# Kernel tuning notes

Hardware: AMD Instinct MI355X
Metric: run time of the kernel (lower is better)

Reference implementation:

```python
import jax, jax.numpy as jnp
import numpy as np

B, G, D, H, KD, E = 64, 512, 128, 8, 16, 128
NS = 20  # num_station


def _init_w(key, shape):
    stdv = 1.0 / np.sqrt(shape[-1]).astype(np.float32)
    return jax.random.uniform(key, shape, jnp.float32, -stdv, stdv)


def setup_inputs() -> dict:
    key = jax.random.key(0)
    ks = jax.random.split(key, 12)
    return {
        "q": jax.random.normal(ks[0], (B, G, D), jnp.float32),
        "h": jax.random.normal(ks[1], (B, G, D), jnp.float32),
        "W_query_depot": _init_w(ks[2], (H, D, KD)),
        "W_key_custom": _init_w(ks[3], (H, D, KD)),
        "W_val_custom": _init_w(ks[4], (H, D, KD)),
        "W_query_station": _init_w(ks[5], (H, D, KD)),
        "W_key_other": _init_w(ks[6], (H, D, KD)),
        "W_val_other": _init_w(ks[7], (H, D, KD)),
        "W_query_custom": _init_w(ks[8], (H, D, KD)),
        "W_key_all": _init_w(ks[9], (H, D, KD)),
        "W_val_all": _init_w(ks[10], (H, D, KD)),
        "W_out": _init_w(ks[11], (H, KD, E)),
        "num_station": NS,
    }


def _mha_block(q_seg, h_seg, Wq, Wk, Wv, norm):
    # q_seg: [B, Nq, D], h_seg: [B, Nk, D]; weights: [H, D, KD]
    Q = jnp.einsum('bqd,hdk->hbqk', q_seg, Wq)
    K = jnp.einsum('bnd,hdk->hbnk', h_seg, Wk)
    V = jnp.einsum('bnd,hdk->hbnk', h_seg, Wv)
    attn = jax.nn.softmax(norm * jnp.einsum('hbqk,hbnk->hbqn', Q, K), axis=-1)
    return jnp.einsum('hbqn,hbnk->hbqk', attn, V)  # [H, B, Nq, KD]


def reference(q, h, W_query_depot, W_key_custom, W_val_custom,
              W_query_station, W_key_other, W_val_other,
              W_query_custom, W_key_all, W_val_all, W_out, num_station):
    ns = num_station
    norm = 1.0 / np.sqrt(W_query_depot.shape[-1]).astype(np.float32)
    h_custom = h[:, 1 + ns:]                                        # customers
    h_other = jnp.concatenate([h[:, :1], h[:, 1 + ns:]], axis=1)    # depot + customers
    heads_depot = _mha_block(q[:, :1], h_custom,
                             W_query_depot, W_key_custom, W_val_custom, norm)
    heads_station = _mha_block(q[:, 1:1 + ns], h_other,
                               W_query_station, W_key_other, W_val_other, norm)
    heads_custom = _mha_block(q[:, 1 + ns:], h,
                              W_query_custom, W_key_all, W_val_all, norm)
    heads = jnp.concatenate([heads_depot, heads_station, heads_custom], axis=2)
    # final projection: mm([B*G, H*KD], [H*KD, E])
    return jnp.einsum('hbgk,hke->bge', heads, W_out)
```

## Files before the change

### kernel.cpp

```cpp
#include <hip/hip_runtime.h>
#include <hip/hip_bf16.h>

namespace {

typedef _Float16 v4h __attribute__((ext_vector_type(4)));
typedef __fp16   h2  __attribute__((ext_vector_type(2)));
typedef float    v4f __attribute__((ext_vector_type(4)));

constexpr int B = 64, G = 512, D = 128, H = 8, KD = 16, NS = 20;
constexpr float NORM = 0.25f;
constexpr float L2E  = 1.44269504088896f;
constexpr float MFIX = 16.0f;
constexpr int KP = 20;
constexpr int VP = 520;

constexpr size_t SZr(int r) { return (size_t)B * H * r * 16; }
constexpr size_t OFF_Q    = 0;
constexpr size_t OFF_K0   = OFF_Q  + SZr(512);
constexpr size_t OFF_V0   = OFF_K0 + SZr(491);
constexpr size_t OFF_K1   = OFF_V0 + SZr(491);
constexpr size_t OFF_V1   = OFF_K1 + SZr(492);
constexpr size_t OFF_K2   = OFF_V1 + SZr(492);
constexpr size_t OFF_V2   = OFF_K2 + SZr(512);
constexpr size_t OFF_FRAG = OFF_V2 + SZr(512);

__device__ __forceinline__ v4f mfma16(v4h a, v4h b, v4f c) {
  return __builtin_amdgcn_mfma_f32_16x16x16f16(a, b, c, 0, 0, 0);
}
__device__ __forceinline__ v4h cvt4(float4 v) {
  h2 a = __builtin_amdgcn_cvt_pkrtz(v.x, v.y);
  h2 b = __builtin_amdgcn_cvt_pkrtz(v.z, v.w);
  return v4h{(_Float16)a[0], (_Float16)a[1], (_Float16)b[0], (_Float16)b[1]};
}
__device__ __forceinline__ v4h cvtacc(v4f v) {
  h2 a = __builtin_amdgcn_cvt_pkrtz(v[0], v[1]);
  h2 b = __builtin_amdgcn_cvt_pkrtz(v[2], v[3]);
  return v4h{(_Float16)a[0], (_Float16)a[1], (_Float16)b[0], (_Float16)b[1]};
}
__device__ __forceinline__ void pexp(v4f s0, v4f s1, v4h& p0, v4h& p1) {
  h2 e01 = __builtin_amdgcn_cvt_pkrtz(__builtin_amdgcn_exp2f(s0[0]),
                                      __builtin_amdgcn_exp2f(s0[1]));
  h2 e23 = __builtin_amdgcn_cvt_pkrtz(__builtin_amdgcn_exp2f(s0[2]),
                                      __builtin_amdgcn_exp2f(s0[3]));
  h2 e45 = __builtin_amdgcn_cvt_pkrtz(__builtin_amdgcn_exp2f(s1[0]),
                                      __builtin_amdgcn_exp2f(s1[1]));
  h2 e67 = __builtin_amdgcn_cvt_pkrtz(__builtin_amdgcn_exp2f(s1[2]),
                                      __builtin_amdgcn_exp2f(s1[3]));
  p0 = {(_Float16)e01[0], (_Float16)e01[1], (_Float16)e23[0], (_Float16)e23[1]};
  p1 = {(_Float16)e45[0], (_Float16)e45[1], (_Float16)e67[0], (_Float16)e67[1]};
}

__global__ __launch_bounds__(256)
void wprep_kernel(const float* __restrict__ Wkc, const float* __restrict__ Wvc,
                  const float* __restrict__ Wko, const float* __restrict__ Wvo,
                  const float* __restrict__ Wka, const float* __restrict__ Wva,
                  const float* __restrict__ Wqc, const float* __restrict__ Wqs,
                  const float* __restrict__ Wqd, _Float16* __restrict__ ws)
{
  const int m = blockIdx.x >> 3;
  const int h = blockIdx.x & 7;
  const float* W;
  float sc = 1.f;
  switch (m) {
    case 0: W = Wkc; break;  case 1: W = Wvc; break;
    case 2: W = Wko; break;  case 3: W = Wvo; break;
    case 4: W = Wka; break;  case 5: W = Wva; break;
    case 6: W = Wqc; sc = NORM * L2E; break;
    case 7: W = Wqs; sc = NORM * L2E; break;
    default: W = Wqd; sc = NORM * L2E; break;
  }
  #pragma unroll
  for (int it = 0; it < 2; ++it) {
    int idx = threadIdx.x + it * 256;
    int dc = idx >> 6, lane = idx & 63, g = lane >> 4, c = lane & 15;
    v4h out;
    #pragma unroll
    for (int i = 0; i < 4; ++i)
      out[i] = (_Float16)(W[((size_t)h * D + dc * 16 + 4 * g + i) * KD + c] * sc);
    *(v4h*)(ws + OFF_FRAG + (((size_t)(m * 8 + h) * 8 + dc) * 64 + lane) * 4) = out;
  }
}

__global__ __launch_bounds__(512)
void proj_kernel(const float* __restrict__ q, const float* __restrict__ hb,
                 _Float16* __restrict__ ws)
{
  const int rt   = blockIdx.x;
  const int b    = blockIdx.y;
  const int tid  = threadIdx.x;
  const int w    = tid >> 6;
  const int lane = tid & 63;
  const int g    = lane >> 4, c = lane & 15;

  __shared__ char ht[16384];

  #pragma unroll
  for (int i = 0; i < 4; ++i) {
    int idx = tid + i * 512, r = idx >> 5, jj = idx & 31;
    float4 v = ((const float4*)(hb + ((size_t)b * G + rt * 64 + r) * D))[jj];
    *(v4h*)(ht + r * 256 + ((8 * jj) ^ ((r & 7) << 4))) = cvt4(v);
  }
  __syncthreads();

  {
    constexpr size_t DOFF[6] = {OFF_K0, OFF_V0, OFF_K1, OFF_V1, OFF_K2, OFF_V2};
    constexpr int    DR[6]   = {491, 491, 492, 492, 512, 512};
    #pragma unroll
    for (int m = 0; m < 6; ++m) {
      v4h wf[8];
      #pragma unroll
      for (int dc = 0; dc < 8; ++dc)
        wf[dc] = *(const v4h*)(ws + OFF_FRAG +
                               (((size_t)(m * 8 + w) * 8 + dc) * 64 + lane) * 4);
      _Float16* dst = ws + DOFF[m] + (size_t)(b * H + w) * (DR[m] * 16);
      const int se = m >> 1;
      #pragma unroll
      for (int s = 0; s < 4; ++s) {
        v4f acc = {0.f, 0.f, 0.f, 0.f};
        #pragma unroll
        for (int dc = 0; dc < 8; ++dc) {
          const v4h a = *(const v4h*)(ht + (s * 16 + c) * 256 +
                                      ((32 * dc + 8 * g) ^ ((c & 7) << 4)));
          acc = mfma16(wf[dc], a, acc);
        }
        v4h out = cvtacc(acc);
        const int hr = rt * 64 + s * 16 + c;
        int n; bool valid;
        if (se == 2)      { n = hr; valid = true; }
        else if (se == 1) { valid = (hr == 0) || (hr >= 1 + NS);
                            n = (hr == 0) ? 0 : hr - NS; }
        else              { valid = (hr >= 1 + NS); n = hr - 1 - NS; }
        if (valid) *(v4h*)(dst + (size_t)n * 16 + 4 * g) = out;
      }
    }
  }

  __syncthreads();
  #pragma unroll
  for (int i = 0; i < 4; ++i) {
    int idx = tid + i * 512, r = idx >> 5, jj = idx & 31;
    float4 v = ((const float4*)(q + ((size_t)b * G + rt * 64 + r) * D))[jj];
    *(v4h*)(ht + r * 256 + ((8 * jj) ^ ((r & 7) << 4))) = cvt4(v);
  }
  __syncthreads();
  {
    auto qproj = [&](int mfrag, int s) -> v4h {
      v4h wf[8];
      #pragma unroll
      for (int dc = 0; dc < 8; ++dc)
        wf[dc] = *(const v4h*)(ws + OFF_FRAG +
                               (((size_t)(mfrag * 8 + w) * 8 + dc) * 64 + lane) * 4);
      v4f acc = {0.f, 0.f, 0.f, 0.f};
      #pragma unroll
      for (int dc = 0; dc < 8; ++dc) {
        const v4h a = *(const v4h*)(ht + (s * 16 + c) * 256 +
                                    ((32 * dc + 8 * g) ^ ((c & 7) << 4)));
        acc = mfma16(wf[dc], a, acc);
      }
      return cvtacc(acc);
    };
    _Float16* dst = ws + OFF_Q + (size_t)(b * H + w) * 512 * 16;
    #pragma unroll
    for (int s = 0; s < 4; ++s) {
      v4h out = qproj(6, s);
      if (rt == 0 && s < 2) {
        const int gq = s * 16 + c;
        v4h outS = qproj(7, s);
        if (s == 0) {
          v4h outD = qproj(8, 0);
          out = (gq == 0) ? outD : (gq <= NS ? outS : out);
        } else {
          out = (gq <= NS) ? outS : out;
        }
      }
      *(v4h*)(dst + (size_t)(rt * 64 + s * 16 + c) * 16 + 4 * g) = out;
    }
  }
}

struct SMA {
  _Float16  Kl[512 * KP];
  _Float16  Vt[16 * VP];
};

template<int SEG, bool PAIR>
__device__ __forceinline__ void attn_loop(const SMA& sm, int g, int c,
                                          v4h qfA, v4h qfB,
                                          v4f& oA, v4f& laA, v4f& oB, v4f& laB)
{
  constexpr int Ln  = SEG == 0 ? G - 1 - NS : SEG == 1 ? G - NS : G;
  constexpr int NCH = (Ln + 31) / 32;
  const _Float16* Kb = sm.Kl + c * KP + 4 * g;
  const _Float16* Vb = sm.Vt + c * VP + 4 * g;
  const v4f mc = {-MFIX, -MFIX, -MFIX, -MFIX};
  const v4h ones = {(_Float16)1.f, (_Float16)1.f, (_Float16)1.f, (_Float16)1.f};

  v4h k0 = *(const v4h*)(Kb);
  v4h k1 = *(const v4h*)(Kb + 16 * KP);
  v4f s0A = mfma16(k0, qfA, mc), s1A = mfma16(k1, qfA, mc);
  v4f s0B, s1B;
  if constexpr (PAIR) { s0B = mfma16(k0, qfB, mc); s1B = mfma16(k1, qfB, mc); }

  #pragma unroll
  for (int ch = 0; ch < NCH; ++ch) {
    const int nb = ch * 32;
    const v4h v0 = *(const v4h*)(Vb + nb);
    const v4h v1 = *(const v4h*)(Vb + nb + 16);
    v4f n0A, n1A, n0B, n1B;
    if (ch + 1 < NCH) {
      k0 = *(const v4h*)(Kb + (nb + 32) * KP);
      k1 = *(const v4h*)(Kb + (nb + 48) * KP);
      n0A = mfma16(k0, qfA, mc); n1A = mfma16(k1, qfA, mc);
      if constexpr (PAIR) { n0B = mfma16(k0, qfB, mc); n1B = mfma16(k1, qfB, mc); }
    }
    if constexpr ((Ln & 31) != 0) {
      if (ch == NCH - 1) {
        #pragma unroll
        for (int r = 0; r < 4; ++r) {
          if (nb + 4 * g + r >= Ln)      { s0A[r] = -1e30f; if constexpr (PAIR) s0B[r] = -1e30f; }
          if (nb + 16 + 4 * g + r >= Ln) { s1A[r] = -1e30f; if constexpr (PAIR) s1B[r] = -1e30f; }
        }
      }
    }
    v4h p0, p1;
    pexp(s0A, s1A, p0, p1);
    oA  = mfma16(v0, p0, oA);
    oA  = mfma16(v1, p1, oA);
    laA = mfma16(ones, p0, laA);
    laA = mfma16(ones, p1, laA);
    if constexpr (PAIR) {
      pexp(s0B, s1B, p0, p1);
      oB  = mfma16(v0, p0, oB);
      oB  = mfma16(v1, p1, oB);
      laB = mfma16(ones, p0, laB);
      laB = mfma16(ones, p1, laB);
      s0B = n0B; s1B = n1B;
    }
    s0A = n0A; s1A = n1A;
  }
}

template<int SEG>
__device__ __forceinline__ void seg_attn(int bid, const _Float16* __restrict__ ws,
                                         float* __restrict__ heads, SMA& sm)
{
  constexpr int Lq   = SEG == 0 ? 1 : SEG == 1 ? NS : G - 1 - NS;
  constexpr int QOFF = SEG == 0 ? 0 : SEG == 1 ? 1  : 1 + NS;
  constexpr int Ln   = SEG == 0 ? G - 1 - NS : SEG == 1 ? G - NS : G;
  constexpr int NQT  = (Lq + 15) / 16;
  constexpr size_t KO = SEG == 0 ? OFF_K0 : SEG == 1 ? OFF_K1 : OFF_K2;
  constexpr size_t VO = SEG == 0 ? OFF_V0 : SEG == 1 ? OFF_V1 : OFF_V2;

  const int hh   = bid >> 6;
  const int b    = bid & 63;
  const int tid  = threadIdx.x;
  const int w    = tid >> 6;
  const int lane = tid & 63;
  const int g    = lane >> 4, c = lane & 15;

  const _Float16* Kws = ws + KO + (size_t)(b * H + hh) * (Ln * 16);
  const _Float16* Vws = ws + VO + (size_t)(b * H + hh) * (Ln * 16);
  const _Float16* Qws = ws + OFF_Q + (size_t)(b * H + hh) * 512 * 16;

  {
    const int n = tid;
    float4 kA = ((const float4*)(Kws + (size_t)n * 16))[0];
    float4 kB = ((const float4*)(Kws + (size_t)n * 16))[1];
    v4h kk[4];
    *(float4*)&kk[0] = kA; *(float4*)&kk[2] = kB;
    #pragma unroll
    for (int i = 0; i < 4; ++i)
      *(v4h*)(sm.Kl + n * KP + 4 * i) = kk[i];
    float4 vA = ((const float4*)(Vws + (size_t)n * 16))[0];
    float4 vB = ((const float4*)(Vws + (size_t)n * 16))[1];
    _Float16 vt[16];
    *(float4*)&vt[0] = vA; *(float4*)&vt[8] = vB;
    #pragma unroll
    for (int k = 0; k < 16; ++k)
      sm.Vt[k * VP + n] = vt[k];
  }
  __syncthreads();

  #pragma unroll
  for (int ps = 0; ps < 2; ++ps) {
    const int t0 = w + 16 * ps, tB = w + 8 + 16 * ps;
    if (t0 >= NQT) continue;
    const bool hasB = tB < NQT;
    v4h qfA = *(const v4h*)(Qws + (size_t)(QOFF + t0 * 16 + c) * 16 + 4 * g);
    v4h qfB = hasB ? *(const v4h*)(Qws + (size_t)(QOFF + tB * 16 + c) * 16 + 4 * g) : qfA;
    v4f oA = {0.f,0.f,0.f,0.f}, laA = {0.f,0.f,0.f,0.f};
    v4f oB = {0.f,0.f,0.f,0.f}, laB = {0.f,0.f,0.f,0.f};
    if (hasB) attn_loop<SEG, true >(sm, g, c, qfA, qfB, oA, laA, oB, laB);
    else      attn_loop<SEG, false>(sm, g, c, qfA, qfA, oA, laA, oB, laB);
    {
      const float inv = 1.0f / laA[0];
      const int qloc = t0 * 16 + c;
      if (qloc < Lq) {
        float4 val = {oA[0]*inv, oA[1]*inv, oA[2]*inv, oA[3]*inv};
        *(float4*)(heads + ((size_t)b * G + QOFF + qloc) * 128 + hh * 16 + 4 * g) = val;
      }
    }
    if (hasB) {
      const float inv = 1.0f / laB[0];
      const int qloc = tB * 16 + c;
      if (qloc < Lq) {
        float4 val = {oB[0]*inv, oB[1]*inv, oB[2]*inv, oB[3]*inv};
        *(float4*)(heads + ((size_t)b * G + QOFF + qloc) * 128 + hh * 16 + 4 * g) = val;
      }
    }
  }
}

__global__ __launch_bounds__(512, 4)
void fused_attn(const _Float16* __restrict__ ws, float* __restrict__ heads)
{
  __shared__ SMA sm;
  const int bid = blockIdx.x;
  if (bid < 512)       seg_attn<2>(bid,        ws, heads, sm);
  else if (bid < 1024) seg_attn<1>(bid - 512,  ws, heads, sm);
  else                 seg_attn<0>(bid - 1024, ws, heads, sm);
}

__global__ __launch_bounds__(256)
void out_proj_kernel(float* __restrict__ data, const float* __restrict__ Wout)
{
  __shared__ _Float16 WlT[128 * 132];
  __shared__ _Float16 Ah [64 * 132];
  const int tid  = threadIdx.x;
  const int lane = tid & 63, w = tid >> 6;
  const int g = lane >> 4, c = lane & 15;
  const size_t rowbase = (size_t)blockIdx.x * 64;

  #pragma unroll
  for (int i = 0; i < 16; ++i) {
    int idx = tid + i * 256;
    int k = idx >> 5, c4 = (idx & 31) * 4;
    float4 v = ((const float4*)Wout)[idx];
    WlT[(c4 + 0) * 132 + k] = (_Float16)v.x;
    WlT[(c4 + 1) * 132 + k] = (_Float16)v.y;
    WlT[(c4 + 2) * 132 + k] = (_Float16)v.z;
    WlT[(c4 + 3) * 132 + k] = (_Float16)v.w;
  }
  #pragma unroll
  for (int i = 0; i < 8; ++i) {
    int idx = tid + i * 256;
    int r = idx >> 5, c4 = (idx & 31) * 4;
    float4 v = ((const float4*)(data + rowbase * 128))[idx];
    *(v4h*)(Ah + r * 132 + c4) = cvt4(v);
  }
  __syncthreads();

  v4h af[8];
  #pragma unroll
  for (int dc = 0; dc < 8; ++dc)
    af[dc] = *(const v4h*)(Ah + (w * 16 + c) * 132 + dc * 16 + 4 * g);
  #pragma unroll
  for (int ct = 0; ct < 8; ++ct) {
    v4f acc = {0.f, 0.f, 0.f, 0.f};
    #pragma unroll
    for (int dc = 0; dc < 8; ++dc) {
      const v4h bf = *(const v4h*)(WlT + (ct * 16 + c) * 132 + dc * 16 + 4 * g);
      acc = mfma16(af[dc], bf, acc);
    }
    #pragma unroll
    for (int r = 0; r < 4; ++r)
      data[(rowbase + w * 16 + 4 * g + r) * 128 + ct * 16 + c] = acc[r];
  }
}

}

extern "C" void kernel_launch(void* const* d_in, const int* in_sizes, int n_in,
                              void* d_out, int out_size, void* d_ws, size_t ws_size,
                              hipStream_t stream) {
  const float* q    = (const float*)d_in[0];
  const float* h    = (const float*)d_in[1];
  const float* Wqd  = (const float*)d_in[2];
  const float* Wkc  = (const float*)d_in[3];
  const float* Wvc  = (const float*)d_in[4];
  const float* Wqs  = (const float*)d_in[5];
  const float* Wko  = (const float*)d_in[6];
  const float* Wvo  = (const float*)d_in[7];
  const float* Wqc  = (const float*)d_in[8];
  const float* Wka  = (const float*)d_in[9];
  const float* Wva  = (const float*)d_in[10];
  const float* Wout = (const float*)d_in[11];
  float* out = (float*)d_out;
  _Float16* ws = (_Float16*)d_ws;

  wprep_kernel<<<72, 256, 0, stream>>>(Wkc, Wvc, Wko, Wvo, Wka, Wva,
                                       Wqc, Wqs, Wqd, ws);
  proj_kernel<<<dim3(8, B), 512, 0, stream>>>(q, h, ws);
  fused_attn<<<3 * B * H, 512, 0, stream>>>(ws, out);
  out_proj_kernel<<<G * B / 64, 256, 0, stream>>>(out, Wout);
}
```

Baseline: 78.63 us.

## Split projection grid finer and process four query tiles per K/V chunk

The projection kernel now runs 256-thread blocks over 32-row tiles and splits the 8 heads across two grid z-slices, which quadruples the block count. The cost is that each h/q tile is loaded and converted twice. The attention loop is restructured so each wave holds up to four query fragments and reads each K/V chunk from shared memory once for all of them. This replaces the paired A/B loop and its software-pipelined K prefetch, cutting LDS reads, but raises register pressure and drops the explicit prefetch.

```diff
diff --git a/kernel.cpp b/kernel.cpp
--- a/kernel.cpp
+++ b/kernel.cpp
@@ -81,23 +81,25 @@
   }
 }
 
-__global__ __launch_bounds__(512)
+__global__ __launch_bounds__(256)
 void proj_kernel(const float* __restrict__ q, const float* __restrict__ hb,
                  _Float16* __restrict__ ws)
 {
   const int rt   = blockIdx.x;
   const int b    = blockIdx.y;
+  const int hz   = blockIdx.z;
   const int tid  = threadIdx.x;
   const int w    = tid >> 6;
+  const int hh   = hz * 4 + w;
   const int lane = tid & 63;
   const int g    = lane >> 4, c = lane & 15;
 
-  __shared__ char ht[16384];
+  __shared__ char ht[8192];
 
   #pragma unroll
   for (int i = 0; i < 4; ++i) {
-    int idx = tid + i * 512, r = idx >> 5, jj = idx & 31;
-    float4 v = ((const float4*)(hb + ((size_t)b * G + rt * 64 + r) * D))[jj];
+    int idx = tid + i * 256, r = idx >> 5, jj = idx & 31;
+    float4 v = ((const float4*)(hb + ((size_t)b * G + rt * 32 + r) * D))[jj];
     *(v4h*)(ht + r * 256 + ((8 * jj) ^ ((r & 7) << 4))) = cvt4(v);
   }
   __syncthreads();
@@ -111,11 +113,11 @@
       #pragma unroll
       for (int dc = 0; dc < 8; ++dc)
         wf[dc] = *(const v4h*)(ws + OFF_FRAG +
-                               (((size_t)(m * 8 + w) * 8 + dc) * 64 + lane) * 4);
-      _Float16* dst = ws + DOFF[m] + (size_t)(b * H + w) * (DR[m] * 16);
+                               (((size_t)(m * 8 + hh) * 8 + dc) * 64 + lane) * 4);
+      _Float16* dst = ws + DOFF[m] + (size_t)(b * H + hh) * (DR[m] * 16);
       const int se = m >> 1;
       #pragma unroll
-      for (int s = 0; s < 4; ++s) {
+      for (int s = 0; s < 2; ++s) {
         v4f acc = {0.f, 0.f, 0.f, 0.f};
         #pragma unroll
         for (int dc = 0; dc < 8; ++dc) {
@@ -124,7 +126,7 @@
           acc = mfma16(wf[dc], a, acc);
         }
         v4h out = cvtacc(acc);
-        const int hr = rt * 64 + s * 16 + c;
+        const int hr = rt * 32 + s * 16 + c;
         int n; bool valid;
         if (se == 2)      { n = hr; valid = true; }
         else if (se == 1) { valid = (hr == 0) || (hr >= 1 + NS);
@@ -138,8 +140,8 @@
   __syncthreads();
   #pragma unroll
   for (int i = 0; i < 4; ++i) {
-    int idx = tid + i * 512, r = idx >> 5, jj = idx & 31;
-    float4 v = ((const float4*)(q + ((size_t)b * G + rt * 64 + r) * D))[jj];
+    int idx = tid + i * 256, r = idx >> 5, jj = idx & 31;
+    float4 v = ((const float4*)(q + ((size_t)b * G + rt * 32 + r) * D))[jj];
     *(v4h*)(ht + r * 256 + ((8 * jj) ^ ((r & 7) << 4))) = cvt4(v);
   }
   __syncthreads();
@@ -149,7 +151,7 @@
       #pragma unroll
       for (int dc = 0; dc < 8; ++dc)
         wf[dc] = *(const v4h*)(ws + OFF_FRAG +
-                               (((size_t)(mfrag * 8 + w) * 8 + dc) * 64 + lane) * 4);
+                               (((size_t)(mfrag * 8 + hh) * 8 + dc) * 64 + lane) * 4);
       v4f acc = {0.f, 0.f, 0.f, 0.f};
       #pragma unroll
       for (int dc = 0; dc < 8; ++dc) {
@@ -159,11 +161,11 @@
       }
       return cvtacc(acc);
     };
-    _Float16* dst = ws + OFF_Q + (size_t)(b * H + w) * 512 * 16;
-    #pragma unroll
-    for (int s = 0; s < 4; ++s) {
+    _Float16* dst = ws + OFF_Q + (size_t)(b * H + hh) * 512 * 16;
+    #pragma unroll
+    for (int s = 0; s < 2; ++s) {
       v4h out = qproj(6, s);
-      if (rt == 0 && s < 2) {
+      if (rt == 0) {
         const int gq = s * 16 + c;
         v4h outS = qproj(7, s);
         if (s == 0) {
@@ -173,7 +175,7 @@
           out = (gq <= NS) ? outS : out;
         }
       }
-      *(v4h*)(dst + (size_t)(rt * 64 + s * 16 + c) * 16 + 4 * g) = out;
+      *(v4h*)(dst + (size_t)(rt * 32 + s * 16 + c) * 16 + 4 * g) = out;
     }
   }
 }
@@ -183,63 +185,6 @@
   _Float16  Vt[16 * VP];
 };
 
-template<int SEG, bool PAIR>
-__device__ __forceinline__ void attn_loop(const SMA& sm, int g, int c,
-                                          v4h qfA, v4h qfB,
-                                          v4f& oA, v4f& laA, v4f& oB, v4f& laB)
-{
-  constexpr int Ln  = SEG == 0 ? G - 1 - NS : SEG == 1 ? G - NS : G;
-  constexpr int NCH = (Ln + 31) / 32;
-  const _Float16* Kb = sm.Kl + c * KP + 4 * g;
-  const _Float16* Vb = sm.Vt + c * VP + 4 * g;
-  const v4f mc = {-MFIX, -MFIX, -MFIX, -MFIX};
-  const v4h ones = {(_Float16)1.f, (_Float16)1.f, (_Float16)1.f, (_Float16)1.f};
-
-  v4h k0 = *(const v4h*)(Kb);
-  v4h k1 = *(const v4h*)(Kb + 16 * KP);
-  v4f s0A = mfma16(k0, qfA, mc), s1A = mfma16(k1, qfA, mc);
-  v4f s0B, s1B;
-  if constexpr (PAIR) { s0B = mfma16(k0, qfB, mc); s1B = mfma16(k1, qfB, mc); }
-
-  #pragma unroll
-  for (int ch = 0; ch < NCH; ++ch) {
-    const int nb = ch * 32;
-    const v4h v0 = *(const v4h*)(Vb + nb);
-    const v4h v1 = *(const v4h*)(Vb + nb + 16);
-    v4f n0A, n1A, n0B, n1B;
-    if (ch + 1 < NCH) {
-      k0 = *(const v4h*)(Kb + (nb + 32) * KP);
-      k1 = *(const v4h*)(Kb + (nb + 48) * KP);
-      n0A = mfma16(k0, qfA, mc); n1A = mfma16(k1, qfA, mc);
-      if constexpr (PAIR) { n0B = mfma16(k0, qfB, mc); n1B = mfma16(k1, qfB, mc); }
-    }
-    if constexpr ((Ln & 31) != 0) {
-      if (ch == NCH - 1) {
-        #pragma unroll
-        for (int r = 0; r < 4; ++r) {
-          if (nb + 4 * g + r >= Ln)      { s0A[r] = -1e30f; if constexpr (PAIR) s0B[r] = -1e30f; }
-          if (nb + 16 + 4 * g + r >= Ln) { s1A[r] = -1e30f; if constexpr (PAIR) s1B[r] = -1e30f; }
-        }
-      }
-    }
-    v4h p0, p1;
-    pexp(s0A, s1A, p0, p1);
-    oA  = mfma16(v0, p0, oA);
-    oA  = mfma16(v1, p1, oA);
-    laA = mfma16(ones, p0, laA);
-    laA = mfma16(ones, p1, laA);
-    if constexpr (PAIR) {
-      pexp(s0B, s1B, p0, p1);
-      oB  = mfma16(v0, p0, oB);
-      oB  = mfma16(v1, p1, oB);
-      laB = mfma16(ones, p0, laB);
-      laB = mfma16(ones, p1, laB);
-      s0B = n0B; s1B = n1B;
-    }
-    s0A = n0A; s1A = n1A;
-  }
-}
-
 template<int SEG>
 __device__ __forceinline__ void seg_attn(int bid, const _Float16* __restrict__ ws,
                                          float* __restrict__ heads, SMA& sm)
@@ -247,6 +192,7 @@
   constexpr int Lq   = SEG == 0 ? 1 : SEG == 1 ? NS : G - 1 - NS;
   constexpr int QOFF = SEG == 0 ? 0 : SEG == 1 ? 1  : 1 + NS;
   constexpr int Ln   = SEG == 0 ? G - 1 - NS : SEG == 1 ? G - NS : G;
+  constexpr int NCH  = (Ln + 31) / 32;
   constexpr int NQT  = (Lq + 15) / 16;
   constexpr size_t KO = SEG == 0 ? OFF_K0 : SEG == 1 ? OFF_K1 : OFF_K2;
   constexpr size_t VO = SEG == 0 ? OFF_V0 : SEG == 1 ? OFF_V1 : OFF_V2;
@@ -281,30 +227,57 @@
   }
   __syncthreads();
 
-  #pragma unroll
-  for (int ps = 0; ps < 2; ++ps) {
-    const int t0 = w + 16 * ps, tB = w + 8 + 16 * ps;
-    if (t0 >= NQT) continue;
-    const bool hasB = tB < NQT;
-    v4h qfA = *(const v4h*)(Qws + (size_t)(QOFF + t0 * 16 + c) * 16 + 4 * g);
-    v4h qfB = hasB ? *(const v4h*)(Qws + (size_t)(QOFF + tB * 16 + c) * 16 + 4 * g) : qfA;
-    v4f oA = {0.f,0.f,0.f,0.f}, laA = {0.f,0.f,0.f,0.f};
-    v4f oB = {0.f,0.f,0.f,0.f}, laB = {0.f,0.f,0.f,0.f};
-    if (hasB) attn_loop<SEG, true >(sm, g, c, qfA, qfB, oA, laA, oB, laB);
-    else      attn_loop<SEG, false>(sm, g, c, qfA, qfA, oA, laA, oB, laB);
-    {
-      const float inv = 1.0f / laA[0];
-      const int qloc = t0 * 16 + c;
+  v4h qf[4] = {};
+  #pragma unroll
+  for (int j = 0; j < 4; ++j) {
+    const int t = w + 8 * j;
+    if (t < NQT)
+      qf[j] = *(const v4h*)(Qws + (size_t)(QOFF + t * 16 + c) * 16 + 4 * g);
+  }
+
+  const _Float16* Kb = sm.Kl + c * KP + 4 * g;
+  const _Float16* Vb = sm.Vt + c * VP + 4 * g;
+  const v4f mc = {-MFIX, -MFIX, -MFIX, -MFIX};
+  const v4h ones = {(_Float16)1.f, (_Float16)1.f, (_Float16)1.f, (_Float16)1.f};
+  v4f o[4]  = {{0.f,0.f,0.f,0.f},{0.f,0.f,0.f,0.f},{0.f,0.f,0.f,0.f},{0.f,0.f,0.f,0.f}};
+  v4f la[4] = {{0.f,0.f,0.f,0.f},{0.f,0.f,0.f,0.f},{0.f,0.f,0.f,0.f},{0.f,0.f,0.f,0.f}};
+  #pragma unroll
+  for (int ch = 0; ch < NCH; ++ch) {
+    const int nb = ch * 32;
+    const v4h k0 = *(const v4h*)(Kb + nb * KP);
+    const v4h k1 = *(const v4h*)(Kb + (nb + 16) * KP);
+    const v4h v0 = *(const v4h*)(Vb + nb);
+    const v4h v1 = *(const v4h*)(Vb + nb + 16);
+    #pragma unroll
+    for (int j = 0; j < 4; ++j) {
+      if (w + 8 * j < NQT) {
+        v4f s0 = mfma16(k0, qf[j], mc);
+        v4f s1 = mfma16(k1, qf[j], mc);
+        if constexpr ((Ln & 31) != 0) {
+          if (ch == NCH - 1) {
+            #pragma unroll
+            for (int r = 0; r < 4; ++r) {
+              if (nb + 4 * g + r >= Ln)      s0[r] = -1e30f;
+              if (nb + 16 + 4 * g + r >= Ln) s1[r] = -1e30f;
+            }
+          }
+        }
+        v4h p0, p1;
+        pexp(s0, s1, p0, p1);
+        o[j]  = mfma16(v0, p0, o[j]);
+        o[j]  = mfma16(v1, p1, o[j]);
+        la[j] = mfma16(ones, p0, la[j]);
+        la[j] = mfma16(ones, p1, la[j]);
+      }
+    }
+  }
+  #pragma unroll
+  for (int j = 0; j < 4; ++j) {
+    if (w + 8 * j < NQT) {
+      const float inv = 1.0f / la[j][0];
+      const int qloc = (w + 8 * j) * 16 + c;
       if (qloc < Lq) {
-        float4 val = {oA[0]*inv, oA[1]*inv, oA[2]*inv, oA[3]*inv};
-        *(float4*)(heads + ((size_t)b * G + QOFF + qloc) * 128 + hh * 16 + 4 * g) = val;
-      }
-    }
-    if (hasB) {
-      const float inv = 1.0f / laB[0];
-      const int qloc = tB * 16 + c;
-      if (qloc < Lq) {
-        float4 val = {oB[0]*inv, oB[1]*inv, oB[2]*inv, oB[3]*inv};
+        float4 val = {o[j][0]*inv, o[j][1]*inv, o[j][2]*inv, o[j][3]*inv};
         *(float4*)(heads + ((size_t)b * G + QOFF + qloc) * 128 + hh * 16 + 4 * g) = val;
       }
     }
@@ -390,7 +363,7 @@
 
   wprep_kernel<<<72, 256, 0, stream>>>(Wkc, Wvc, Wko, Wvo, Wka, Wva,
                                        Wqc, Wqs, Wqd, ws);
-  proj_kernel<<<dim3(8, B), 512, 0, stream>>>(q, h, ws);
+  proj_kernel<<<dim3(16, B, 2), 256, 0, stream>>>(q, h, ws);
   fused_attn<<<3 * B * H, 512, 0, stream>>>(ws, out);
   out_proj_kernel<<<G * B / 64, 256, 0, stream>>>(out, Wout);
 }
```

New measurement: 74.58 us. 1.05x faster.
